# Kernel optimization log

Measured on AMD Instinct MI355X. Metric: run time of the kernel, lower is better.

## Reference

```python
import jax, jax.numpy as jnp
import numpy as np

B, S, E = 4, 2048, 1024
H, DK = 16, 64

def setup_inputs() -> dict:
    key = jax.random.key(0)
    ks = jax.random.split(key, 9)
    sc = 1.0 / np.sqrt(E)
    return {
        "q": jax.random.normal(ks[0], (B, S, E), jnp.float32),
        "Wq": jax.random.normal(ks[1], (E, H * DK), jnp.float32) * sc,
        "bq": jax.random.normal(ks[2], (H * DK,), jnp.float32) * 0.01,
        "Wk": jax.random.normal(ks[3], (E, H * DK), jnp.float32) * sc,
        "bk": jax.random.normal(ks[4], (H * DK,), jnp.float32) * 0.01,
        "Wv": jax.random.normal(ks[5], (E, H * DK), jnp.float32) * sc,
        "bv": jax.random.normal(ks[6], (H * DK,), jnp.float32) * 0.01,
        "Wo": jax.random.normal(ks[7], (H * DK, E), jnp.float32) * sc,
        "bo": jax.random.normal(ks[8], (E,), jnp.float32) * 0.01,
    }

def _split_heads(x):
    # (B, S, H*DK) -> (B, H, S, DK)
    return x.reshape(B, S, H, DK).transpose(0, 2, 1, 3)

def reference(q, Wq, bq, Wk, bk, Wv, bv, Wo, bo):
    # self-attention: k = v = q (torch module path when k=v=None)
    qh = _split_heads(q @ Wq + bq)
    kh = _split_heads(q @ Wk + bk)
    vh = _split_heads(q @ Wv + bv)
    scale = 1.0 / jnp.sqrt(jnp.asarray(DK, qh.dtype))
    scores = jnp.einsum("bhqd,bhkd->bhqk", qh, kh) * scale  # (B,H,S,S)
    attn = jax.nn.softmax(scores, axis=-1)
    ctx = jnp.einsum("bhqk,bhkd->bhqd", attn, vh)
    ctx = ctx.transpose(0, 2, 1, 3).reshape(B, S, H * DK)
    return ctx @ Wo + bo
```

## Files before the change

kernel.cpp:

```cpp
#include <hip/hip_runtime.h>
#include <hip/hip_bf16.h>
#include <math.h>


typedef _Float16 f16x8 __attribute__((ext_vector_type(8)));
typedef _Float16 f16x4 __attribute__((ext_vector_type(4)));
typedef _Float16 f16x2 __attribute__((ext_vector_type(2)));
typedef float    f32x4 __attribute__((ext_vector_type(4)));
typedef unsigned int u32x2 __attribute__((ext_vector_type(2)));
typedef unsigned int u32x4 __attribute__((ext_vector_type(4)));

#define MFMA16(a,b,c) __builtin_amdgcn_mfma_f32_16x16x32_f16(a,b,c,0,0,0)

__device__ __forceinline__ void async_cp16(const _Float16* g, _Float16* l) {
    __builtin_amdgcn_global_load_lds(
        (const __attribute__((address_space(1))) unsigned int*)g,
        (__attribute__((address_space(3))) unsigned int*)l,
        16, 0, 0);
}

__device__ __forceinline__ f16x2 pk(float a, float b) {
    return __builtin_bit_cast(f16x2, __builtin_amdgcn_cvt_pkrtz(a, b));
}

__global__ void __launch_bounds__(256) prep(
    const float* __restrict__ X,
    const float* __restrict__ Wq, const float* __restrict__ Wk,
    const float* __restrict__ Wv, const float* __restrict__ Wo,
    _Float16* __restrict__ Xh, _Float16* __restrict__ wt)
{
    __shared__ float tile[32][33];
    const int bx = blockIdx.x;
    if (bx < 8192) {
        int i = (bx*256 + threadIdx.x)*4;
        f32x4 x = *(const f32x4*)&X[i];
        f16x4 h;
        #pragma unroll
        for (int k=0;k<4;k++) h[k] = (_Float16)x[k];
        *(f16x4*)&Xh[i] = h;
        return;
    }
    int t = bx - 8192;
    int mat = t >> 10;
    int tloc = t & 1023;
    const float* W = (mat==0)?Wq:(mat==1)?Wk:(mat==2)?Wv:Wo;
    _Float16* WT = wt + (size_t)mat*1048576;
    int kb = (tloc & 31) * 32;
    int nb = (tloc >> 5) * 32;
    int tx = threadIdx.x & 31, ty = threadIdx.x >> 5;
    #pragma unroll
    for (int r = 0; r < 4; ++r) {
        int row = ty + r*8;
        tile[row][tx] = W[(size_t)(kb+row)*1024 + nb + tx];
    }
    __syncthreads();
    #pragma unroll
    for (int r = 0; r < 4; ++r) {
        int row = ty + r*8;
        WT[(size_t)(nb+row)*1024 + kb + tx] = (_Float16)tile[tx][row];
    }
}

__device__ __forceinline__ void stage3a(
    const _Float16* __restrict__ Ag, const _Float16* __restrict__ Bg, int kb,
    _Float16* sAb, _Float16* sBb, int wave, int lane)
{
    #pragma unroll
    for (int j = 0; j < 2; ++j) {
        int d   = j*512 + wave*64 + lane;
        int row = d >> 3;
        int sg  = (d & 7) ^ (row & 7);
        async_cp16(&Ag[(size_t)row*1024 + kb + sg*8], sAb + (j*512 + wave*64)*8);
    }
    {
        int d   = wave*64 + lane;
        int row = d >> 3;
        int sg  = (d & 7) ^ (row & 7);
        async_cp16(&Bg[(size_t)row*1024 + kb + sg*8], sBb + (wave*64)*8);
    }
}
__device__ __forceinline__ void stage3b(
    const _Float16* __restrict__ Bg, int kb, _Float16* sBb, int wave, int lane)
{
    #pragma unroll
    for (int j = 1; j < 4; ++j) {
        int d   = j*512 + wave*64 + lane;
        int row = d >> 3;
        int sg  = (d & 7) ^ (row & 7);
        async_cp16(&Bg[(size_t)row*1024 + kb + sg*8], sBb + (j*512 + wave*64)*8);
    }
}

#define GEMM_PIPE_LOOP()                                                       \
    stage3a(Ag, Bg, 0,  pA0, pB0, wave, lane);                                 \
    stage3b(Bg, 0,  pB0, wave, lane);                                          \
    stage3a(Ag, Bg, 64, pA1, pB1, wave, lane);                                 \
    stage3b(Bg, 64, pB1, wave, lane);                                          \
    asm volatile("s_waitcnt vmcnt(6)" ::: "memory");                           \
    __builtin_amdgcn_s_barrier();                                              \
    __builtin_amdgcn_sched_barrier(0);                                         \
    for (int t = 0; t < 16; ++t) {                                             \
        f16x8 af0[4], bf0[4];                                                  \
        _Pragma("unroll")                                                      \
        for (int i = 0; i < 4; ++i)                                            \
            af0[i] = *(const f16x8*)&pA0[(wr*64+i*16+cc)*64 +                  \
                                         ((q4^(cc&7))*8)];                     \
        _Pragma("unroll")                                                      \
        for (int j = 0; j < 4; ++j)                                            \
            bf0[j] = *(const f16x8*)&pB0[(wc*64+j*16+cc)*64 +                  \
                                         ((q4^(cc&7))*8)];                     \
        if (t < 14) stage3a(Ag, Bg, (t+2)*64, pA2, pB2, wave, lane);           \
        __builtin_amdgcn_sched_barrier(0);                                     \
        __builtin_amdgcn_s_barrier();                                          \
        asm volatile("s_waitcnt lgkmcnt(0)" ::: "memory");                     \
        __builtin_amdgcn_sched_barrier(0);                                     \
        __builtin_amdgcn_s_setprio(1);                                         \
        _Pragma("unroll")                                                      \
        for (int i = 0; i < 4; ++i)                                            \
            _Pragma("unroll")                                                  \
            for (int j = 0; j < 4; ++j)                                        \
                acc[i][j] = MFMA16(af0[i], bf0[j], acc[i][j]);                 \
        __builtin_amdgcn_s_setprio(0);                                         \
        __builtin_amdgcn_sched_barrier(0);                                     \
        __builtin_amdgcn_s_barrier();                                          \
        f16x8 af1[4], bf1[4];                                                  \
        _Pragma("unroll")                                                      \
        for (int i = 0; i < 4; ++i)                                            \
            af1[i] = *(const f16x8*)&pA0[(wr*64+i*16+cc)*64 +                  \
                                         (((4+q4)^(cc&7))*8)];                 \
        _Pragma("unroll")                                                      \
        for (int j = 0; j < 4; ++j)                                            \
            bf1[j] = *(const f16x8*)&pB0[(wc*64+j*16+cc)*64 +                  \
                                         (((4+q4)^(cc&7))*8)];                 \
        if (t < 14) stage3b(Bg, (t+2)*64, pB2, wave, lane);                    \
        __builtin_amdgcn_sched_barrier(0);                                     \
        __builtin_amdgcn_s_barrier();                                          \
        asm volatile("s_waitcnt lgkmcnt(0)" ::: "memory");                     \
        __builtin_amdgcn_sched_barrier(0);                                     \
        __builtin_amdgcn_s_setprio(1);                                         \
        _Pragma("unroll")                                                      \
        for (int i = 0; i < 4; ++i)                                            \
            _Pragma("unroll")                                                  \
            for (int j = 0; j < 4; ++j)                                        \
                acc[i][j] = MFMA16(af1[i], bf1[j], acc[i][j]);                 \
        __builtin_amdgcn_s_setprio(0);                                         \
        if (t < 14) asm volatile("s_waitcnt vmcnt(6)" ::: "memory");           \
        else        asm volatile("s_waitcnt vmcnt(0)" ::: "memory");           \
        __builtin_amdgcn_sched_barrier(0);                                     \
        __builtin_amdgcn_s_barrier();                                          \
        _Float16* tA = pA0; pA0 = pA1; pA1 = pA2; pA2 = tA;                    \
        _Float16* tB = pB0; pB0 = pB1; pB1 = pB2; pB2 = tB;                    \
    }

__global__ void __launch_bounds__(512) gemm_qkv(
    const _Float16* __restrict__ Xh, const _Float16* __restrict__ wt,
    const float* __restrict__ bq, const float* __restrict__ bk, const float* __restrict__ bv,
    _Float16* __restrict__ Q, _Float16* __restrict__ K, _Float16* __restrict__ Vt)
{
    __shared__ __align__(16) _Float16 sA[3][8192];
    __shared__ __align__(16) _Float16 sB[3][16384];

    const int id = blockIdx.x;
    const int xcd = id & 7;
    const int lid = id >> 3;
    const int ng  = lid >> 5;
    const int rem = lid & 31;
    const int mq  = rem >> 4;
    const int r2  = rem & 15;
    const int m_lo = r2 >> 2;
    const int nb   = r2 & 3;
    const int mblk = (mq*4 + m_lo)*8 + xcd;
    const int nblk = ng*4 + nb;

    const int tid = threadIdx.x;
    const int wave = tid >> 6, lane = tid & 63;
    const int wr = wave & 1, wc = wave >> 1;
    const int q4 = lane >> 4, cc = lane & 15;

    const int mat = nblk >> 2;
    const int colbase = (nblk & 3) * 256;
    const _Float16* Bg = wt + (size_t)mat*1048576 + (size_t)colbase*1024;
    const _Float16* Ag = Xh + (size_t)mblk*131072;

    _Float16 *pA0 = &sA[0][0], *pA1 = &sA[1][0], *pA2 = &sA[2][0];
    _Float16 *pB0 = &sB[0][0], *pB1 = &sB[1][0], *pB2 = &sB[2][0];

    f32x4 acc[4][4] = {};

    GEMM_PIPE_LOOP()

    const float* bias = (mat==0)?bq:(mat==1)?bk:bv;
    const float QSCALE = 0.125f * 1.44269504f;
    #pragma unroll
    for (int i=0;i<4;i++)
      #pragma unroll
      for (int j=0;j<4;j++)
        #pragma unroll
        for (int r=0;r<4;r++){
            int m = mblk*128 + wr*64 + i*16 + q4*4 + r;
            int ncol = colbase + wc*64 + j*16 + cc;
            float val = acc[i][j][r] + bias[ncol];
            int b = m >> 11, s = m & 2047;
            int h = ncol >> 6, dk = ncol & 63;
            if (mat == 2) {
                Vt[((size_t)(b*16+h)*64 + dk)*2048 + s] = (_Float16)val;
            } else {
                size_t qi = ((size_t)(b*16+h)*2048 + s)*64 + dk;
                if (mat == 0) Q[qi] = (_Float16)(val * QSCALE);
                else          K[qi] = (_Float16)val;
            }
        }
}

__global__ void __launch_bounds__(512) gemm_out(
    const _Float16* __restrict__ Ctx, const _Float16* __restrict__ wt,
    const float* __restrict__ bo,
    float* __restrict__ out)
{
    __shared__ __align__(16) _Float16 sA[3][8192];
    __shared__ __align__(16) _Float16 sB[3][16384];

    const int id = blockIdx.x;
    const int xcd = id & 7;
    const int lid = id >> 3;
    const int mq  = lid >> 4;
    const int r2  = lid & 15;
    const int m_lo = r2 >> 2;
    const int nblk = r2 & 3;
    const int mblk = (mq*4 + m_lo)*8 + xcd;

    const int tid = threadIdx.x;
    const int wave = tid >> 6, lane = tid & 63;
    const int wr = wave & 1, wc = wave >> 1;
    const int q4 = lane >> 4, cc = lane & 15;

    const _Float16* Bg = wt + (size_t)3*1048576 + (size_t)nblk*256*1024;
    const _Float16* Ag = Ctx + (size_t)mblk*131072;

    _Float16 *pA0 = &sA[0][0], *pA1 = &sA[1][0], *pA2 = &sA[2][0];
    _Float16 *pB0 = &sB[0][0], *pB1 = &sB[1][0], *pB2 = &sB[2][0];

    f32x4 acc[4][4] = {};

    GEMM_PIPE_LOOP()

    #pragma unroll
    for (int i=0;i<4;i++)
      #pragma unroll
      for (int j=0;j<4;j++)
        #pragma unroll
        for (int r=0;r<4;r++){
            int m = mblk*128 + wr*64 + i*16 + q4*4 + r;
            int n = nblk*256 + wc*64 + j*16 + cc;
            out[(size_t)m*1024 + n] = acc[i][j][r] + bo[n];
        }
}

__global__ void __launch_bounds__(256,4) attn(
    const _Float16* __restrict__ Qg, const _Float16* __restrict__ Kg,
    const _Float16* __restrict__ Vg,
    _Float16* __restrict__ Ctx)
{
    __shared__ __align__(16) _Float16 sK[2][4096];
    __shared__ __align__(16) _Float16 sV[2][4096];

    const int id = blockIdx.x;
    const int xcd = id & 7;
    const int t2 = id >> 3;
    const int qc = t2 & 15;
    const int bh = (t2 >> 4) * 8 + xcd;

    const int tid = threadIdx.x;
    const int wave = tid >> 6, lane = tid & 63;
    const int q4 = lane >> 4, cc = lane & 15;

    const size_t hoff = (size_t)bh * 131072;
    const _Float16* Qp = Qg + hoff;
    const _Float16* Kp = Kg + hoff;
    const _Float16* Vp = Vg + hoff;

    const int qbase = qc*128 + wave*32;

    f16x8 qf[2][2];
    #pragma unroll
    for (int m=0;m<2;m++)
      #pragma unroll
      for (int ks=0;ks<2;ks++)
        qf[m][ks] = *(const f16x8*)&Qp[(qbase+m*16+cc)*64 + ks*32 + q4*8];

    f16x8 vones;
    #pragma unroll
    for (int k=0;k<8;k++) vones[k] = (_Float16)1.0f;

    f32x4 o[2][4] = {};
    f32x4 oL[2] = {};

    const int srow = tid >> 3;
    const int scg  = ((tid & 7) ^ ((tid >> 3) & 7)) * 8;
    int kofs[2], vofs[2], dofs[2];
    #pragma unroll
    for (int rr = 0; rr < 2; ++rr) {
        kofs[rr] = (rr*32 + srow)*64 + scg;
        vofs[rr] = (rr*32 + srow)*2048 + scg;
        dofs[rr] = rr*2048 + wave*512;
    }
    int okA[4], okB[4];
    #pragma unroll
    for (int kj=0;kj<4;kj++){
        okA[kj] = (kj*16+cc)*64 + ((q4    ^(cc&7))*8);
        okB[kj] = (kj*16+cc)*64 + (((4+q4)^(cc&7))*8);
    }
    int ov[2][4];
    #pragma unroll
    for (int ks=0;ks<2;ks++)
      #pragma unroll
      for (int v=0;v<4;v++)
        ov[ks][v] = (v*16+cc)*64 + (((ks*4+q4)^(cc&7))*8);

    #pragma unroll
    for (int rr = 0; rr < 2; ++rr) {
        async_cp16(Kp + kofs[rr], &sK[0][dofs[rr]]);
        async_cp16(Vp + vofs[rr], &sV[0][dofs[rr]]);
    }
    asm volatile("s_waitcnt vmcnt(0)" ::: "memory");
    __syncthreads();
    __builtin_amdgcn_sched_barrier(0);

    const _Float16* KbN = Kp + 4096;
    const _Float16* VbN = Vp + 64;

    #pragma unroll 2
    for (int kt = 0; kt < 32; ++kt) {
        const int cur = kt & 1;
        const _Float16* kc = &sK[cur][0];
        const _Float16* vc = &sV[cur][0];

        if (kt < 31) {
            _Float16* kn = &sK[cur ^ 1][0];
            _Float16* vn = &sV[cur ^ 1][0];
            #pragma unroll
            for (int rr = 0; rr < 2; ++rr) {
                async_cp16(KbN + kofs[rr], kn + dofs[rr]);
                async_cp16(VbN + vofs[rr], vn + dofs[rr]);
            }
        }

        #pragma unroll
        for (int ks=0;ks<2;ks++){
            unsigned Ud[2][2], Wd[2][2];
            #pragma unroll
            for (int aa=0;aa<2;aa++){
                int kj = ks*2 + aa;
                f16x8 k0 = *(const f16x8*)&kc[okA[kj]];
                f16x8 k1 = *(const f16x8*)&kc[okB[kj]];
                #pragma unroll
                for (int m=0;m<2;m++){
                    f32x4 z = {};
                    f32x4 s = MFMA16(k0, qf[m][0], z);
                    s = MFMA16(k1, qf[m][1], s);
                    float p0 = __builtin_amdgcn_exp2f(s[0]);
                    float p1 = __builtin_amdgcn_exp2f(s[1]);
                    float p2 = __builtin_amdgcn_exp2f(s[2]);
                    float p3 = __builtin_amdgcn_exp2f(s[3]);
                    unsigned d0 = __builtin_bit_cast(unsigned, pk(p0, p1));
                    unsigned d1 = __builtin_bit_cast(unsigned, pk(p2, p3));
                    if (aa == 0) { Ud[m][0] = d0; Ud[m][1] = d1; }
                    else         { Wd[m][0] = d0; Wd[m][1] = d1; }
                }
            }
            f16x8 pa[2];
            #pragma unroll
            for (int m=0;m<2;m++){
                u32x2 x0 = __builtin_amdgcn_permlane32_swap(Ud[m][0], Wd[m][0], false, false);
                u32x2 r02 = __builtin_amdgcn_permlane16_swap(x0[0], x0[1], false, false);
                u32x2 x1 = __builtin_amdgcn_permlane32_swap(Ud[m][1], Wd[m][1], false, false);
                u32x2 r13 = __builtin_amdgcn_permlane16_swap(x1[0], x1[1], false, false);
                u32x4 pw;
                pw[0] = r02[0]; pw[1] = r13[0]; pw[2] = r02[1]; pw[3] = r13[1];
                pa[m] = __builtin_bit_cast(f16x8, pw);
            }
            #pragma unroll
            for (int v=0;v<4;v++){
                f16x8 vf = *(const f16x8*)&vc[ov[ks][v]];
                o[0][v] = MFMA16(pa[0], vf, o[0][v]);
                o[1][v] = MFMA16(pa[1], vf, o[1][v]);
            }
            oL[0] = MFMA16(pa[0], vones, oL[0]);
            oL[1] = MFMA16(pa[1], vones, oL[1]);
        }

        KbN += 4096;
        VbN += 64;
        asm volatile("s_waitcnt vmcnt(0)" ::: "memory");
        __syncthreads();
        __builtin_amdgcn_sched_barrier(0);
    }

    int b = bh >> 4, h = bh & 15;
    #pragma unroll
    for (int m=0;m<2;m++)
      #pragma unroll
      for (int r=0;r<4;r++){
        float inv = 1.f / oL[m][r];
        int s = qbase + m*16 + q4*4 + r;
        #pragma unroll
        for (int v=0;v<4;v++){
            float val = o[m][v][r]*inv;
            int dk = v*16 + cc;
            Ctx[((size_t)(b*2048+s)*16 + h)*64 + dk] = (_Float16)val;
        }
      }
}

extern "C" void kernel_launch(void* const* d_in, const int* in_sizes, int n_in,
                              void* d_out, int out_size, void* d_ws, size_t ws_size,
                              hipStream_t stream)
{
    const float* q  = (const float*)d_in[0];
    const float* Wq = (const float*)d_in[1];
    const float* bq = (const float*)d_in[2];
    const float* Wk = (const float*)d_in[3];
    const float* bk = (const float*)d_in[4];
    const float* Wv = (const float*)d_in[5];
    const float* bv = (const float*)d_in[6];
    const float* Wo = (const float*)d_in[7];
    const float* bo = (const float*)d_in[8];
    float* out = (float*)d_out;

    _Float16* ws  = (_Float16*)d_ws;
    _Float16* wt  = ws;
    _Float16* Xh  = ws + 4194304;
    _Float16* Q   = ws + 12582912;
    _Float16* K   = ws + 20971520;
    _Float16* Vt  = ws + 29360128;
    _Float16* Ctx = Xh;

    prep<<<dim3(12288), 256, 0, stream>>>(q, Wq, Wk, Wv, Wo, Xh, wt);
    gemm_qkv<<<dim3(768), 512, 0, stream>>>(Xh, wt, bq, bk, bv, Q, K, Vt);
    attn<<<dim3(1024), 256, 0, stream>>>(Q, K, Vt, Ctx);
    gemm_out<<<dim3(256), 512, 0, stream>>>(Ctx, wt, bo, out);
}
```

Baseline: 274.1 us.

## Enlarge GEMM tiles to 256x256 with simple double-buffered K loop

Both projection GEMMs now use 256x256 output tiles with 8 waves (2x4), each wave computing 128x64, replacing the 128x256 tiles with the triple-buffered, split-stage pipeline. The K loop becomes a plain double buffer that waits with vmcnt(0) and a barrier every iteration, and launch bounds request two blocks per CU. Grid sizes halve (384 and 128 blocks). Larger tiles raise operand reuse per LDS byte, but the coarser pipeline exposes load latency. Halving the block count also leaves gemm_out with fewer blocks than CUs, and gemm_qkv with just over one block per CU, so load balance gets worse.

```diff
diff --git a/kernel.cpp b/kernel.cpp
--- a/kernel.cpp
+++ b/kernel.cpp
@@ -61,143 +61,112 @@
     }
 }
 
-__device__ __forceinline__ void stage3a(
-    const _Float16* __restrict__ Ag, const _Float16* __restrict__ Bg, int kb,
-    _Float16* sAb, _Float16* sBb, int wave, int lane)
-{
-    #pragma unroll
-    for (int j = 0; j < 2; ++j) {
-        int d   = j*512 + wave*64 + lane;
+__device__ __forceinline__ void stage256(
+    const _Float16* __restrict__ g, _Float16* l, int tid)
+{
+    #pragma unroll
+    for (int j = 0; j < 4; ++j) {
+        int d   = j*512 + tid;
         int row = d >> 3;
         int sg  = (d & 7) ^ (row & 7);
-        async_cp16(&Ag[(size_t)row*1024 + kb + sg*8], sAb + (j*512 + wave*64)*8);
-    }
-    {
-        int d   = wave*64 + lane;
-        int row = d >> 3;
-        int sg  = (d & 7) ^ (row & 7);
-        async_cp16(&Bg[(size_t)row*1024 + kb + sg*8], sBb + (wave*64)*8);
-    }
-}
-__device__ __forceinline__ void stage3b(
-    const _Float16* __restrict__ Bg, int kb, _Float16* sBb, int wave, int lane)
-{
-    #pragma unroll
-    for (int j = 1; j < 4; ++j) {
-        int d   = j*512 + wave*64 + lane;
-        int row = d >> 3;
-        int sg  = (d & 7) ^ (row & 7);
-        async_cp16(&Bg[(size_t)row*1024 + kb + sg*8], sBb + (j*512 + wave*64)*8);
-    }
-}
-
-#define GEMM_PIPE_LOOP()                                                       \
-    stage3a(Ag, Bg, 0,  pA0, pB0, wave, lane);                                 \
-    stage3b(Bg, 0,  pB0, wave, lane);                                          \
-    stage3a(Ag, Bg, 64, pA1, pB1, wave, lane);                                 \
-    stage3b(Bg, 64, pB1, wave, lane);                                          \
-    asm volatile("s_waitcnt vmcnt(6)" ::: "memory");                           \
+        async_cp16(&g[(size_t)row*1024 + sg*8], l + d*8);
+    }
+}
+
+#define GEMM_K_LOOP_256()                                                      \
+    stage256(Ag, &sA[0][0], tid);                                              \
+    stage256(Bg, &sB[0][0], tid);                                              \
+    asm volatile("s_waitcnt vmcnt(0)" ::: "memory");                           \
     __builtin_amdgcn_s_barrier();                                              \
     __builtin_amdgcn_sched_barrier(0);                                         \
-    for (int t = 0; t < 16; ++t) {                                             \
-        f16x8 af0[4], bf0[4];                                                  \
-        _Pragma("unroll")                                                      \
-        for (int i = 0; i < 4; ++i)                                            \
-            af0[i] = *(const f16x8*)&pA0[(wr*64+i*16+cc)*64 +                  \
-                                         ((q4^(cc&7))*8)];                     \
-        _Pragma("unroll")                                                      \
-        for (int j = 0; j < 4; ++j)                                            \
-            bf0[j] = *(const f16x8*)&pB0[(wc*64+j*16+cc)*64 +                  \
-                                         ((q4^(cc&7))*8)];                     \
-        if (t < 14) stage3a(Ag, Bg, (t+2)*64, pA2, pB2, wave, lane);           \
-        __builtin_amdgcn_sched_barrier(0);                                     \
-        __builtin_amdgcn_s_barrier();                                          \
-        asm volatile("s_waitcnt lgkmcnt(0)" ::: "memory");                     \
-        __builtin_amdgcn_sched_barrier(0);                                     \
-        __builtin_amdgcn_s_setprio(1);                                         \
-        _Pragma("unroll")                                                      \
-        for (int i = 0; i < 4; ++i)                                            \
+    {                                                                          \
+        const _Float16* AgN = Ag + 64;                                         \
+        const _Float16* BgN = Bg + 64;                                         \
+        const int abase0 = (wr*128 + cc)*64 + ((q4    ^(cc&7))*8);             \
+        const int abase1 = (wr*128 + cc)*64 + (((4+q4)^(cc&7))*8);             \
+        const int bbase0 = (wc*64  + cc)*64 + ((q4    ^(cc&7))*8);             \
+        const int bbase1 = (wc*64  + cc)*64 + (((4+q4)^(cc&7))*8);             \
+        _Pragma("unroll 2")                                                    \
+        for (int t = 0; t < 16; ++t) {                                         \
+            const int cur = t & 1;                                             \
+            const _Float16* ka = &sA[cur][0];                                  \
+            const _Float16* kb_ = &sB[cur][0];                                 \
+            if (t < 15) {                                                      \
+                stage256(AgN, &sA[cur^1][0], tid);                             \
+                stage256(BgN, &sB[cur^1][0], tid);                             \
+            }                                                                  \
+            f16x8 af[8], bf[4];                                                \
+            _Pragma("unroll")                                                  \
+            for (int i = 0; i < 8; ++i)                                        \
+                af[i] = *(const f16x8*)&ka[abase0 + i*1024];                   \
             _Pragma("unroll")                                                  \
             for (int j = 0; j < 4; ++j)                                        \
-                acc[i][j] = MFMA16(af0[i], bf0[j], acc[i][j]);                 \
-        __builtin_amdgcn_s_setprio(0);                                         \
-        __builtin_amdgcn_sched_barrier(0);                                     \
-        __builtin_amdgcn_s_barrier();                                          \
-        f16x8 af1[4], bf1[4];                                                  \
-        _Pragma("unroll")                                                      \
-        for (int i = 0; i < 4; ++i)                                            \
-            af1[i] = *(const f16x8*)&pA0[(wr*64+i*16+cc)*64 +                  \
-                                         (((4+q4)^(cc&7))*8)];                 \
-        _Pragma("unroll")                                                      \
-        for (int j = 0; j < 4; ++j)                                            \
-            bf1[j] = *(const f16x8*)&pB0[(wc*64+j*16+cc)*64 +                  \
-                                         (((4+q4)^(cc&7))*8)];                 \
-        if (t < 14) stage3b(Bg, (t+2)*64, pB2, wave, lane);                    \
-        __builtin_amdgcn_sched_barrier(0);                                     \
-        __builtin_amdgcn_s_barrier();                                          \
-        asm volatile("s_waitcnt lgkmcnt(0)" ::: "memory");                     \
-        __builtin_amdgcn_sched_barrier(0);                                     \
-        __builtin_amdgcn_s_setprio(1);                                         \
-        _Pragma("unroll")                                                      \
-        for (int i = 0; i < 4; ++i)                                            \
+                bf[j] = *(const f16x8*)&kb_[bbase0 + j*1024];                  \
+            __builtin_amdgcn_s_setprio(1);                                     \
+            _Pragma("unroll")                                                  \
+            for (int i = 0; i < 8; ++i)                                        \
+                _Pragma("unroll")                                              \
+                for (int j = 0; j < 4; ++j)                                    \
+                    acc[i][j] = MFMA16(af[i], bf[j], acc[i][j]);               \
+            __builtin_amdgcn_s_setprio(0);                                     \
+            _Pragma("unroll")                                                  \
+            for (int i = 0; i < 8; ++i)                                        \
+                af[i] = *(const f16x8*)&ka[abase1 + i*1024];                   \
             _Pragma("unroll")                                                  \
             for (int j = 0; j < 4; ++j)                                        \
-                acc[i][j] = MFMA16(af1[i], bf1[j], acc[i][j]);                 \
-        __builtin_amdgcn_s_setprio(0);                                         \
-        if (t < 14) asm volatile("s_waitcnt vmcnt(6)" ::: "memory");           \
-        else        asm volatile("s_waitcnt vmcnt(0)" ::: "memory");           \
-        __builtin_amdgcn_sched_barrier(0);                                     \
-        __builtin_amdgcn_s_barrier();                                          \
-        _Float16* tA = pA0; pA0 = pA1; pA1 = pA2; pA2 = tA;                    \
-        _Float16* tB = pB0; pB0 = pB1; pB1 = pB2; pB2 = tB;                    \
-    }
-
-__global__ void __launch_bounds__(512) gemm_qkv(
+                bf[j] = *(const f16x8*)&kb_[bbase1 + j*1024];                  \
+            __builtin_amdgcn_s_setprio(1);                                     \
+            _Pragma("unroll")                                                  \
+            for (int i = 0; i < 8; ++i)                                        \
+                _Pragma("unroll")                                              \
+                for (int j = 0; j < 4; ++j)                                    \
+                    acc[i][j] = MFMA16(af[i], bf[j], acc[i][j]);               \
+            __builtin_amdgcn_s_setprio(0);                                     \
+            AgN += 64; BgN += 64;                                              \
+            asm volatile("s_waitcnt vmcnt(0)" ::: "memory");                   \
+            __builtin_amdgcn_s_barrier();                                      \
+            __builtin_amdgcn_sched_barrier(0);                                 \
+        }                                                                      \
+    }
+
+__global__ void __launch_bounds__(512,2) gemm_qkv(
     const _Float16* __restrict__ Xh, const _Float16* __restrict__ wt,
     const float* __restrict__ bq, const float* __restrict__ bk, const float* __restrict__ bv,
     _Float16* __restrict__ Q, _Float16* __restrict__ K, _Float16* __restrict__ Vt)
 {
-    __shared__ __align__(16) _Float16 sA[3][8192];
-    __shared__ __align__(16) _Float16 sB[3][16384];
+    __shared__ __align__(16) _Float16 sA[2][16384];
+    __shared__ __align__(16) _Float16 sB[2][16384];
 
     const int id = blockIdx.x;
     const int xcd = id & 7;
     const int lid = id >> 3;
-    const int ng  = lid >> 5;
-    const int rem = lid & 31;
-    const int mq  = rem >> 4;
-    const int r2  = rem & 15;
-    const int m_lo = r2 >> 2;
-    const int nb   = r2 & 3;
-    const int mblk = (mq*4 + m_lo)*8 + xcd;
-    const int nblk = ng*4 + nb;
+    const int nblk = lid >> 2;
+    const int m_lo = lid & 3;
+    const int mblk = m_lo*8 + xcd;
 
     const int tid = threadIdx.x;
     const int wave = tid >> 6, lane = tid & 63;
-    const int wr = wave & 1, wc = wave >> 1;
+    const int wr = wave >> 2, wc = wave & 3;
     const int q4 = lane >> 4, cc = lane & 15;
 
     const int mat = nblk >> 2;
     const int colbase = (nblk & 3) * 256;
     const _Float16* Bg = wt + (size_t)mat*1048576 + (size_t)colbase*1024;
-    const _Float16* Ag = Xh + (size_t)mblk*131072;
-
-    _Float16 *pA0 = &sA[0][0], *pA1 = &sA[1][0], *pA2 = &sA[2][0];
-    _Float16 *pB0 = &sB[0][0], *pB1 = &sB[1][0], *pB2 = &sB[2][0];
-
-    f32x4 acc[4][4] = {};
-
-    GEMM_PIPE_LOOP()
+    const _Float16* Ag = Xh + (size_t)mblk*262144;
+
+    f32x4 acc[8][4] = {};
+
+    GEMM_K_LOOP_256()
 
     const float* bias = (mat==0)?bq:(mat==1)?bk:bv;
     const float QSCALE = 0.125f * 1.44269504f;
     #pragma unroll
-    for (int i=0;i<4;i++)
+    for (int i=0;i<8;i++)
       #pragma unroll
       for (int j=0;j<4;j++)
         #pragma unroll
         for (int r=0;r<4;r++){
-            int m = mblk*128 + wr*64 + i*16 + q4*4 + r;
+            int m = mblk*256 + wr*128 + i*16 + q4*4 + r;
             int ncol = colbase + wc*64 + j*16 + cc;
             float val = acc[i][j][r] + bias[ncol];
             int b = m >> 11, s = m & 2047;
@@ -212,45 +181,40 @@
         }
 }
 
-__global__ void __launch_bounds__(512) gemm_out(
+__global__ void __launch_bounds__(512,2) gemm_out(
     const _Float16* __restrict__ Ctx, const _Float16* __restrict__ wt,
     const float* __restrict__ bo,
     float* __restrict__ out)
 {
-    __shared__ __align__(16) _Float16 sA[3][8192];
-    __shared__ __align__(16) _Float16 sB[3][16384];
+    __shared__ __align__(16) _Float16 sA[2][16384];
+    __shared__ __align__(16) _Float16 sB[2][16384];
 
     const int id = blockIdx.x;
     const int xcd = id & 7;
     const int lid = id >> 3;
-    const int mq  = lid >> 4;
-    const int r2  = lid & 15;
-    const int m_lo = r2 >> 2;
-    const int nblk = r2 & 3;
-    const int mblk = (mq*4 + m_lo)*8 + xcd;
+    const int nblk = lid >> 2;
+    const int m_lo = lid & 3;
+    const int mblk = m_lo*8 + xcd;
 
     const int tid = threadIdx.x;
     const int wave = tid >> 6, lane = tid & 63;
-    const int wr = wave & 1, wc = wave >> 1;
+    const int wr = wave >> 2, wc = wave & 3;
     const int q4 = lane >> 4, cc = lane & 15;
 
     const _Float16* Bg = wt + (size_t)3*1048576 + (size_t)nblk*256*1024;
-    const _Float16* Ag = Ctx + (size_t)mblk*131072;
-
-    _Float16 *pA0 = &sA[0][0], *pA1 = &sA[1][0], *pA2 = &sA[2][0];
-    _Float16 *pB0 = &sB[0][0], *pB1 = &sB[1][0], *pB2 = &sB[2][0];
-
-    f32x4 acc[4][4] = {};
-
-    GEMM_PIPE_LOOP()
-
-    #pragma unroll
-    for (int i=0;i<4;i++)
+    const _Float16* Ag = Ctx + (size_t)mblk*262144;
+
+    f32x4 acc[8][4] = {};
+
+    GEMM_K_LOOP_256()
+
+    #pragma unroll
+    for (int i=0;i<8;i++)
       #pragma unroll
       for (int j=0;j<4;j++)
         #pragma unroll
         for (int r=0;r<4;r++){
-            int m = mblk*128 + wr*64 + i*16 + q4*4 + r;
+            int m = mblk*256 + wr*128 + i*16 + q4*4 + r;
             int n = nblk*256 + wc*64 + j*16 + cc;
             out[(size_t)m*1024 + n] = acc[i][j][r] + bo[n];
         }
@@ -436,7 +400,7 @@
     _Float16* Ctx = Xh;
 
     prep<<<dim3(12288), 256, 0, stream>>>(q, Wq, Wk, Wv, Wo, Xh, wt);
-    gemm_qkv<<<dim3(768), 512, 0, stream>>>(Xh, wt, bq, bk, bv, Q, K, Vt);
+    gemm_qkv<<<dim3(384), 512, 0, stream>>>(Xh, wt, bq, bk, bv, Q, K, Vt);
     attn<<<dim3(1024), 256, 0, stream>>>(Q, K, Vt, Ctx);
-    gemm_out<<<dim3(256), 512, 0, stream>>>(Ctx, wt, bo, out);
-}
+    gemm_out<<<dim3(128), 512, 0, stream>>>(Ctx, wt, bo, out);
+}
```

After: 376.2 us. +37.2%, slower.
